# Optimization experiments

Hardware: AMD Instinct MI355X
Metric: run time of the kernel (lower is better)

Reference implementation:

```python
import jax, jax.numpy as jnp
import numpy as np

N = 100000      # nodes
E = 1600000     # directed edges (avg degree 16)
D_IN, D_H, D_OUT = 128, 128, 64


def glorot(k, fi, fo):
    s = (6.0 / (fi + fo)) ** 0.5
    return jax.random.uniform(k, (fi, fo), jnp.float32, -s, s)


def setup_inputs() -> dict:
    key = jax.random.key(0)
    ks = jax.random.split(key, 5)
    edges = jax.random.randint(ks[0], (2, E), 0, N)
    features = jax.random.normal(ks[1], (N, D_IN), dtype=jnp.float32)
    return dict(
        edges=edges,
        features=features,
        W0=glorot(ks[2], D_IN, D_H), b0=jnp.zeros((D_H,), jnp.float32),
        W1=glorot(ks[3], D_H, D_H), b1=jnp.zeros((D_H,), jnp.float32),
        W2=glorot(ks[4], D_H, D_OUT), b2=jnp.zeros((D_OUT,), jnp.float32),
    )


def _prep(edges):
    # add self-loops and compute symmetric GCN normalization D^-1/2 A_hat D^-1/2
    loop = jnp.arange(N)
    row = jnp.concatenate([edges[0], loop])  # source
    col = jnp.concatenate([edges[1], loop])  # target
    deg = jax.ops.segment_sum(jnp.ones((row.shape[0],), jnp.float32), col, num_segments=N)
    dinv = jnp.where(deg > 0, jax.lax.rsqrt(deg), 0.0)
    norm = dinv[row] * dinv[col]             # per-edge coefficient
    return row, col, norm


def gcn_conv(x, row, col, norm, W, b):
    x = x @ W                                 # [N, out]
    msg = x[row] * norm[:, None]              # gather + scale, [E+N, out]
    return jax.ops.segment_sum(msg, col, num_segments=N) + b


def reference(edges, features, W0, b0, W1, b1, W2, b2):
    row, col, norm = _prep(edges)
    h = jax.nn.relu(gcn_conv(features, row, col, norm, W0, b0))
    h = jax.nn.relu(gcn_conv(h, row, col, norm, W1, b1))
    h = gcn_conv(h, row, col, norm, W2, b2)
    return jax.nn.log_softmax(h, axis=1)
```

## Files before the change

### kernel.cpp

```cpp
#include <hip/hip_runtime.h>
#include <hip/hip_bf16.h>
#include <math.h>

#define NN 100000
#define EE 1600000
#define NB2 391
#define NPART 256
#define CAP 4736

typedef __attribute__((ext_vector_type(8))) short short8;
typedef __attribute__((ext_vector_type(4))) float f32x4;
typedef __attribute__((ext_vector_type(2))) float f32x2;

__device__ inline unsigned short f2bf(float x) {
    unsigned u = __float_as_uint(x);
    unsigned r = u + 0x7FFFu + ((u >> 16) & 1u);
    return (unsigned short)(r >> 16);
}
__device__ inline unsigned pack2bf(float a, float b) {
    return (unsigned)f2bf(a) | ((unsigned)f2bf(b) << 16);
}
__device__ inline f32x2 bf2f2(unsigned u) {
    f32x2 r;
    r.x = __uint_as_float(u << 16);
    r.y = __uint_as_float(u & 0xFFFF0000u);
    return r;
}


__global__ void prep_weights(const float* __restrict__ W0, const float* __restrict__ W1,
                             const float* __restrict__ W2, unsigned short* __restrict__ Wt0,
                             unsigned short* __restrict__ Wt1, unsigned short* __restrict__ Wt2,
                             int* __restrict__ bcount) {
    int g = blockIdx.x * 256 + threadIdx.x;
    if (g < NB2) bcount[g] = 0;
    if (g < 16384) {
        int n = g >> 7, k = g & 127;
        Wt0[g] = f2bf(W0[k * 128 + n]);
    } else if (g < 32768) {
        int i = g - 16384;
        int n = i >> 7, k = i & 127;
        Wt1[i] = f2bf(W1[k * 128 + n]);
    } else if (g < 40960) {
        int i = g - 32768;
        int n = i >> 7, k = i & 127;
        Wt2[i] = f2bf(W2[k * 64 + n]);
    }
}


__global__ __launch_bounds__(256) void scatter_bump(const int* __restrict__ src,
                                                    const int* __restrict__ dst,
                                                    int* __restrict__ bcount,
                                                    int* __restrict__ P, int e) {
    __shared__ int cnt[NB2];
    __shared__ int basep[NB2];
    __shared__ int cur[NB2];
    int t = threadIdx.x;
    for (int i = t; i < NB2; i += 256) { cnt[i] = 0; cur[i] = 0; }
    __syncthreads();
    int chunk = (e + NPART - 1) / NPART;
    int b0 = blockIdx.x * chunk, b1 = min(e, b0 + chunk);
    for (int i = b0 + t; i < b1; i += 256)
        atomicAdd(&cnt[dst[i] >> 8], 1);
    __syncthreads();
    for (int i = t; i < NB2; i += 256) {
        int c = cnt[i];
        basep[i] = c ? atomicAdd(&bcount[i], c) : 0;
    }
    __syncthreads();
    for (int i = b0 + t; i < b1; i += 256) {
        int d = dst[i];
        int b = d >> 8;
        int p = basep[b] + atomicAdd(&cur[b], 1);
        P[(size_t)b * CAP + p] = (src[i] << 8) | (d & 255);
    }
}

__global__ __launch_bounds__(256) void bucket_build(const int* __restrict__ P,
                                                    const int* __restrict__ bcount,
                                                    int2* __restrict__ offs2,
                                                    float* __restrict__ dinv,
                                                    int* __restrict__ csr, int n) {
    __shared__ int cnt[256];
    __shared__ int sc[256];
    __shared__ int cur[256];
    __shared__ int stage[CAP];
    int b = blockIdx.x, t = threadIdx.x;
    int base = b * CAP;
    int count = bcount[b];
    cnt[t] = 0;
    __syncthreads();
    for (int i = t; i < count; i += 256)
        atomicAdd(&cnt[P[base + i] & 255], 1);
    __syncthreads();
    int v = cnt[t];
    sc[t] = v;
    for (int d = 1; d < 256; d <<= 1) {
        __syncthreads();
        int x = (t >= d) ? sc[t - d] : 0;
        __syncthreads();
        sc[t] += x;
    }
    __syncthreads();
    int myoff = sc[t] - v;
    int node = b * 256 + t;
    if (node < n) {
        offs2[node] = make_int2(base + myoff, base + myoff + v);
        dinv[node] = 1.0f / sqrtf((float)(v + 1));
    }
    cur[t] = myoff;
    __syncthreads();
    for (int i = t; i < count; i += 256) {
        int pe = P[base + i];
        int p = atomicAdd(&cur[pe & 255], 1);
        stage[p] = ((unsigned)pe) >> 8;
    }
    __syncthreads();
    for (int i = t; i < count; i += 256) csr[base + i] = stage[i];
}

template <int DOUT, bool A_IS_F32>
__global__ __launch_bounds__(256) void gemm_mfma(const void* __restrict__ Aptr,
                                                 const unsigned short* __restrict__ Wt,
                                                 const float* __restrict__ dinv,
                                                 unsigned short* __restrict__ Y, int nrows) {
    constexpr int KP = 136;
    constexpr int NT = DOUT / 16;
    __shared__ unsigned short sA[128 * KP];
    __shared__ unsigned short sB[DOUT * KP];
    const int row0 = blockIdx.x * 128;
    const int tid = threadIdx.x;

    for (int i = tid; i < DOUT * 16; i += 256) {
        int n = i >> 4, c = (i & 15) * 8;
        uint4 v = *(const uint4*)(Wt + n * 128 + c);
        *(uint4*)(&sB[n * KP + c]) = v;
    }
    if (A_IS_F32) {
        const float* A = (const float*)Aptr;
        for (int i = tid; i < 128 * 32; i += 256) {
            int r = i >> 5, c = (i & 31) * 4;
            float4 v = make_float4(0.f, 0.f, 0.f, 0.f);
            if (row0 + r < nrows) v = *(const float4*)(A + (size_t)(row0 + r) * 128 + c);
            uint2 o;
            o.x = pack2bf(v.x, v.y);
            o.y = pack2bf(v.z, v.w);
            *(uint2*)(&sA[r * KP + c]) = o;
        }
    } else {
        const unsigned short* A = (const unsigned short*)Aptr;
        for (int i = tid; i < 128 * 16; i += 256) {
            int r = i >> 4, c = (i & 15) * 8;
            uint4 v = make_uint4(0u, 0u, 0u, 0u);
            if (row0 + r < nrows) v = *(const uint4*)(A + (size_t)(row0 + r) * 128 + c);
            *(uint4*)(&sA[r * KP + c]) = v;
        }
    }
    __syncthreads();

    const int wave = tid >> 6;
    const int lane = tid & 63;
    const int m0 = lane & 15;
    const int kq = (lane >> 4) * 8;

    f32x4 acc[2][NT];
#pragma unroll
    for (int rt = 0; rt < 2; ++rt)
#pragma unroll
        for (int t = 0; t < NT; ++t) acc[rt][t] = (f32x4){0.f, 0.f, 0.f, 0.f};

#pragma unroll
    for (int k0 = 0; k0 < 128; k0 += 32) {
        short8 a0 = *(const short8*)(&sA[(wave * 32 + m0) * KP + k0 + kq]);
        short8 a1 = *(const short8*)(&sA[(wave * 32 + 16 + m0) * KP + k0 + kq]);
#pragma unroll
        for (int t = 0; t < NT; ++t) {
            short8 b = *(const short8*)(&sB[(t * 16 + m0) * KP + k0 + kq]);
            acc[0][t] = __builtin_amdgcn_mfma_f32_16x16x32_bf16(a0, b, acc[0][t], 0, 0, 0);
            acc[1][t] = __builtin_amdgcn_mfma_f32_16x16x32_bf16(a1, b, acc[1][t], 0, 0, 0);
        }
    }

#pragma unroll
    for (int rt = 0; rt < 2; ++rt)
#pragma unroll
        for (int r = 0; r < 4; ++r) {
            int row = row0 + wave * 32 + rt * 16 + (lane >> 4) * 4 + r;
            if (row < nrows) {
                float dv = dinv[row];
#pragma unroll
                for (int t = 0; t < NT; ++t)
                    Y[(size_t)row * DOUT + t * 16 + (lane & 15)] = f2bf(acc[rt][t][r] * dv);
            }
        }
}

__global__ __launch_bounds__(256) void agg128_bf16(const unsigned short* __restrict__ Xp,
                                                   const int* __restrict__ csr,
                                                   const int2* __restrict__ offs2,
                                                   const float* __restrict__ dinv,
                                                   const float* __restrict__ bias,
                                                   unsigned short* __restrict__ Y, int n) {
    __shared__ int sIdx[4][64];
    int wv = threadIdx.x >> 6;
    int node = blockIdx.x * 4 + wv;
    if (node >= n) return;
    int lane = threadIdx.x & 63;
    int q = lane >> 4;
    int l = lane & 15;
    int2 se = offs2[node];
    int s = se.x, deg = se.y - se.x;
    if (lane < deg) sIdx[wv][lane] = csr[s + lane];
    int dcap = min(deg, 64);
    const int* idx = sIdx[wv];
    f32x2 a0 = {0.f, 0.f}, a1 = {0.f, 0.f}, a2 = {0.f, 0.f}, a3 = {0.f, 0.f};
    int j = q;
    for (; j + 12 < dcap; j += 16) {
        int s0 = idx[j], s1 = idx[j + 4], s2 = idx[j + 8], s3 = idx[j + 12];
        uint4 u0 = *(const uint4*)(Xp + (size_t)s0 * 128 + l * 8);
        uint4 u1 = *(const uint4*)(Xp + (size_t)s1 * 128 + l * 8);
        uint4 u2 = *(const uint4*)(Xp + (size_t)s2 * 128 + l * 8);
        uint4 u3 = *(const uint4*)(Xp + (size_t)s3 * 128 + l * 8);
        a0 += bf2f2(u0.x); a1 += bf2f2(u0.y); a2 += bf2f2(u0.z); a3 += bf2f2(u0.w);
        a0 += bf2f2(u1.x); a1 += bf2f2(u1.y); a2 += bf2f2(u1.z); a3 += bf2f2(u1.w);
        a0 += bf2f2(u2.x); a1 += bf2f2(u2.y); a2 += bf2f2(u2.z); a3 += bf2f2(u2.w);
        a0 += bf2f2(u3.x); a1 += bf2f2(u3.y); a2 += bf2f2(u3.z); a3 += bf2f2(u3.w);
    }
    for (; j < dcap; j += 4) {
        int s0 = idx[j];
        uint4 u = *(const uint4*)(Xp + (size_t)s0 * 128 + l * 8);
        a0 += bf2f2(u.x); a1 += bf2f2(u.y); a2 += bf2f2(u.z); a3 += bf2f2(u.w);
    }
    for (int p = s + 64 + q; p < s + deg; p += 4) {
        int s0 = csr[p];
        uint4 u = *(const uint4*)(Xp + (size_t)s0 * 128 + l * 8);
        a0 += bf2f2(u.x); a1 += bf2f2(u.y); a2 += bf2f2(u.z); a3 += bf2f2(u.w);
    }
    if (q == 0) {
        uint4 u = *(const uint4*)(Xp + (size_t)node * 128 + l * 8);
        a0 += bf2f2(u.x); a1 += bf2f2(u.y); a2 += bf2f2(u.z); a3 += bf2f2(u.w);
    }
    float r0 = a0.x, r1 = a0.y, r2 = a1.x, r3 = a1.y;
    float r4 = a2.x, r5 = a2.y, r6 = a3.x, r7 = a3.y;
    r0 += __shfl_xor(r0, 16); r0 += __shfl_xor(r0, 32);
    r1 += __shfl_xor(r1, 16); r1 += __shfl_xor(r1, 32);
    r2 += __shfl_xor(r2, 16); r2 += __shfl_xor(r2, 32);
    r3 += __shfl_xor(r3, 16); r3 += __shfl_xor(r3, 32);
    r4 += __shfl_xor(r4, 16); r4 += __shfl_xor(r4, 32);
    r5 += __shfl_xor(r5, 16); r5 += __shfl_xor(r5, 32);
    r6 += __shfl_xor(r6, 16); r6 += __shfl_xor(r6, 32);
    r7 += __shfl_xor(r7, 16); r7 += __shfl_xor(r7, 32);
    if (q == 0) {
        float di = dinv[node];
        float4 bA = *(const float4*)(bias + l * 8);
        float4 bB = *(const float4*)(bias + l * 8 + 4);
        r0 = fmaxf(fmaf(di, r0, bA.x), 0.f); r1 = fmaxf(fmaf(di, r1, bA.y), 0.f);
        r2 = fmaxf(fmaf(di, r2, bA.z), 0.f); r3 = fmaxf(fmaf(di, r3, bA.w), 0.f);
        r4 = fmaxf(fmaf(di, r4, bB.x), 0.f); r5 = fmaxf(fmaf(di, r5, bB.y), 0.f);
        r6 = fmaxf(fmaf(di, r6, bB.z), 0.f); r7 = fmaxf(fmaf(di, r7, bB.w), 0.f);
        uint4 o;
        o.x = pack2bf(r0, r1); o.y = pack2bf(r2, r3);
        o.z = pack2bf(r4, r5); o.w = pack2bf(r6, r7);
        *(uint4*)(Y + (size_t)node * 128 + l * 8) = o;
    }
}

__global__ __launch_bounds__(256) void agg_softmax64_bf16(const unsigned short* __restrict__ Xp,
                                                          const int* __restrict__ csr,
                                                          const int2* __restrict__ offs2,
                                                          const float* __restrict__ dinv,
                                                          const float* __restrict__ bias,
                                                          float* __restrict__ out, int n) {
    __shared__ int sIdx[4][64];
    int wv = threadIdx.x >> 6;
    int node = blockIdx.x * 4 + wv;
    if (node >= n) return;
    int lane = threadIdx.x & 63;
    int g8 = lane >> 3;
    int l = lane & 7;
    int2 se = offs2[node];
    int s = se.x, deg = se.y - se.x;
    if (lane < deg) sIdx[wv][lane] = csr[s + lane];
    int dcap = min(deg, 64);
    const int* idx = sIdx[wv];
    f32x2 a0 = {0.f, 0.f}, a1 = {0.f, 0.f}, a2 = {0.f, 0.f}, a3 = {0.f, 0.f};
    int j = g8;
    for (; j + 8 < dcap; j += 16) {
        int s0 = idx[j], s1 = idx[j + 8];
        uint4 u0 = *(const uint4*)(Xp + (size_t)s0 * 64 + l * 8);
        uint4 u1 = *(const uint4*)(Xp + (size_t)s1 * 64 + l * 8);
        a0 += bf2f2(u0.x); a1 += bf2f2(u0.y); a2 += bf2f2(u0.z); a3 += bf2f2(u0.w);
        a0 += bf2f2(u1.x); a1 += bf2f2(u1.y); a2 += bf2f2(u1.z); a3 += bf2f2(u1.w);
    }
    if (j < dcap) {
        int s0 = idx[j];
        uint4 u = *(const uint4*)(Xp + (size_t)s0 * 64 + l * 8);
        a0 += bf2f2(u.x); a1 += bf2f2(u.y); a2 += bf2f2(u.z); a3 += bf2f2(u.w);
    }
    for (int p = s + 64 + g8; p < s + deg; p += 8) {
        int s0 = csr[p];
        uint4 u = *(const uint4*)(Xp + (size_t)s0 * 64 + l * 8);
        a0 += bf2f2(u.x); a1 += bf2f2(u.y); a2 += bf2f2(u.z); a3 += bf2f2(u.w);
    }
    if (g8 == 0) {
        uint4 u = *(const uint4*)(Xp + (size_t)node * 64 + l * 8);
        a0 += bf2f2(u.x); a1 += bf2f2(u.y); a2 += bf2f2(u.z); a3 += bf2f2(u.w);
    }
    float r0 = a0.x, r1 = a0.y, r2 = a1.x, r3 = a1.y;
    float r4 = a2.x, r5 = a2.y, r6 = a3.x, r7 = a3.y;
    r0 += __shfl_xor(r0, 8); r0 += __shfl_xor(r0, 16); r0 += __shfl_xor(r0, 32);
    r1 += __shfl_xor(r1, 8); r1 += __shfl_xor(r1, 16); r1 += __shfl_xor(r1, 32);
    r2 += __shfl_xor(r2, 8); r2 += __shfl_xor(r2, 16); r2 += __shfl_xor(r2, 32);
    r3 += __shfl_xor(r3, 8); r3 += __shfl_xor(r3, 16); r3 += __shfl_xor(r3, 32);
    r4 += __shfl_xor(r4, 8); r4 += __shfl_xor(r4, 16); r4 += __shfl_xor(r4, 32);
    r5 += __shfl_xor(r5, 8); r5 += __shfl_xor(r5, 16); r5 += __shfl_xor(r5, 32);
    r6 += __shfl_xor(r6, 8); r6 += __shfl_xor(r6, 16); r6 += __shfl_xor(r6, 32);
    r7 += __shfl_xor(r7, 8); r7 += __shfl_xor(r7, 16); r7 += __shfl_xor(r7, 32);
    if (g8 == 0) {
        float di = dinv[node];
        float4 bA = *(const float4*)(bias + l * 8);
        float4 bB = *(const float4*)(bias + l * 8 + 4);
        r0 = fmaf(di, r0, bA.x); r1 = fmaf(di, r1, bA.y);
        r2 = fmaf(di, r2, bA.z); r3 = fmaf(di, r3, bA.w);
        r4 = fmaf(di, r4, bB.x); r5 = fmaf(di, r5, bB.y);
        r6 = fmaf(di, r6, bB.z); r7 = fmaf(di, r7, bB.w);
        float m = fmaxf(fmaxf(fmaxf(r0, r1), fmaxf(r2, r3)), fmaxf(fmaxf(r4, r5), fmaxf(r6, r7)));
#pragma unroll
        for (int o = 4; o > 0; o >>= 1) m = fmaxf(m, __shfl_xor(m, o));
        float ssum = __expf(r0 - m) + __expf(r1 - m) + __expf(r2 - m) + __expf(r3 - m) +
                     __expf(r4 - m) + __expf(r5 - m) + __expf(r6 - m) + __expf(r7 - m);
#pragma unroll
        for (int o = 4; o > 0; o >>= 1) ssum += __shfl_xor(ssum, o);
        float lg = m + __logf(ssum);
        float4 o0 = make_float4(r0 - lg, r1 - lg, r2 - lg, r3 - lg);
        float4 o1 = make_float4(r4 - lg, r5 - lg, r6 - lg, r7 - lg);
        *(float4*)(out + (size_t)node * 64 + l * 8) = o0;
        *(float4*)(out + (size_t)node * 64 + l * 8 + 4) = o1;
    }
}


extern "C" void kernel_launch(void* const* d_in, const int* in_sizes, int n_in,
                              void* d_out, int out_size, void* d_ws, size_t ws_size,
                              hipStream_t stream) {
    const int* edges = (const int*)d_in[0];
    const float* feat = (const float*)d_in[1];
    const float* W0 = (const float*)d_in[2];
    const float* b0 = (const float*)d_in[3];
    const float* W1 = (const float*)d_in[4];
    const float* b1 = (const float*)d_in[5];
    const float* W2 = (const float*)d_in[6];
    const float* b2 = (const float*)d_in[7];

    const int N = NN;
    const int E = EE;

    char* ws = (char*)d_ws;
    int* bcount = (int*)ws;
    int2* offs2 = (int2*)(bcount + ((NB2 + 1) & ~1));
    float* dinv = (float*)(offs2 + N);
    int* P = (int*)(dinv + N);
    int* csr = P + (size_t)NB2 * CAP;
    unsigned short* Wt0 = (unsigned short*)(csr + (size_t)NB2 * CAP);
    unsigned short* Wt1 = Wt0 + 16384;
    unsigned short* Wt2 = Wt1 + 16384;
    size_t off = (size_t)((char*)(Wt2 + 8192) - ws);
    off = (off + 255) & ~(size_t)255;
    unsigned short* bufA = (unsigned short*)(ws + off);
    unsigned short* bufB = bufA + (size_t)N * 128;

    const int* esrc = edges;
    const int* edst = edges + E;

    prep_weights<<<160, 256, 0, stream>>>(W0, W1, W2, Wt0, Wt1, Wt2, bcount);
    scatter_bump<<<NPART, 256, 0, stream>>>(esrc, edst, bcount, P, E);
    bucket_build<<<NB2, 256, 0, stream>>>(P, bcount, offs2, dinv, csr, N);

    const int gemmBlocks = (N + 127) / 128;
    const int aggBlocks = (N + 3) / 4;

    gemm_mfma<128, true><<<gemmBlocks, 256, 0, stream>>>(feat, Wt0, dinv, bufA, N);
    agg128_bf16<<<aggBlocks, 256, 0, stream>>>(bufA, csr, offs2, dinv, b0, bufB, N);
    gemm_mfma<128, false><<<gemmBlocks, 256, 0, stream>>>(bufB, Wt1, dinv, bufA, N);
    agg128_bf16<<<aggBlocks, 256, 0, stream>>>(bufA, csr, offs2, dinv, b1, bufB, N);
    gemm_mfma<64, false><<<gemmBlocks, 256, 0, stream>>>(bufB, Wt2, dinv, bufA, N);
    agg_softmax64_bf16<<<aggBlocks, 256, 0, stream>>>(bufA, csr, offs2, dinv, b2, (float*)d_out, N);
}
```

Measured before the change: 394.7 us.

## Store hidden features in 16-column slices so aggregation gathers fit cache

Hidden activations for the 128-wide layers are now laid out as 8 column slices of 16 bf16 values per node, each slice a contiguous N×16 array. The GEMM writes and reads this sliced layout, and the aggregation kernel launches 8× more blocks, each handling a single slice for 4 nodes. Each slice (about 3.2MB) is small enough to stay resident in L2/LLC during the random neighbour gathers. The cost is 8× redundant CSR/offset reads and index staging, 8-byte gathers instead of 16-byte ones, and more shuffle-reduction steps.

```diff
diff --git a/kernel.cpp b/kernel.cpp
--- a/kernel.cpp
+++ b/kernel.cpp
@@ -7,6 +7,7 @@
 #define NB2 391
 #define NPART 256
 #define CAP 4736
+#define SLS ((size_t)NN * 16)
 
 typedef __attribute__((ext_vector_type(8))) short short8;
 typedef __attribute__((ext_vector_type(4))) float f32x4;
@@ -120,7 +121,7 @@
     for (int i = t; i < count; i += 256) csr[base + i] = stage[i];
 }
 
-template <int DOUT, bool A_IS_F32>
+template <int DOUT, bool A_IS_F32, bool Y_SLICED>
 __global__ __launch_bounds__(256) void gemm_mfma(const void* __restrict__ Aptr,
                                                  const unsigned short* __restrict__ Wt,
                                                  const float* __restrict__ dinv,
@@ -151,10 +152,12 @@
     } else {
         const unsigned short* A = (const unsigned short*)Aptr;
         for (int i = tid; i < 128 * 16; i += 256) {
-            int r = i >> 4, c = (i & 15) * 8;
+            int r = i >> 4, c8 = (i & 15) * 8;
+            int sl = c8 >> 4, inner = c8 & 15;
             uint4 v = make_uint4(0u, 0u, 0u, 0u);
-            if (row0 + r < nrows) v = *(const uint4*)(A + (size_t)(row0 + r) * 128 + c);
-            *(uint4*)(&sA[r * KP + c]) = v;
+            if (row0 + r < nrows)
+                v = *(const uint4*)(A + (size_t)sl * SLS + (size_t)(row0 + r) * 16 + inner);
+            *(uint4*)(&sA[r * KP + c8]) = v;
         }
     }
     __syncthreads();
@@ -190,8 +193,13 @@
             if (row < nrows) {
                 float dv = dinv[row];
 #pragma unroll
-                for (int t = 0; t < NT; ++t)
-                    Y[(size_t)row * DOUT + t * 16 + (lane & 15)] = f2bf(acc[rt][t][r] * dv);
+                for (int t = 0; t < NT; ++t) {
+                    unsigned short val = f2bf(acc[rt][t][r] * dv);
+                    if (Y_SLICED)
+                        Y[(size_t)t * SLS + (size_t)row * 16 + (lane & 15)] = val;
+                    else
+                        Y[(size_t)row * DOUT + t * 16 + (lane & 15)] = val;
+                }
             }
         }
 }
@@ -203,66 +211,62 @@
                                                    const float* __restrict__ bias,
                                                    unsigned short* __restrict__ Y, int n) {
     __shared__ int sIdx[4][64];
+    int slice = blockIdx.x & 7;
+    int group = blockIdx.x >> 3;
     int wv = threadIdx.x >> 6;
-    int node = blockIdx.x * 4 + wv;
+    int node = group * 4 + wv;
     if (node >= n) return;
     int lane = threadIdx.x & 63;
-    int q = lane >> 4;
-    int l = lane & 15;
+    int sub = lane >> 2;
+    int l = lane & 3;
     int2 se = offs2[node];
     int s = se.x, deg = se.y - se.x;
     if (lane < deg) sIdx[wv][lane] = csr[s + lane];
     int dcap = min(deg, 64);
     const int* idx = sIdx[wv];
-    f32x2 a0 = {0.f, 0.f}, a1 = {0.f, 0.f}, a2 = {0.f, 0.f}, a3 = {0.f, 0.f};
-    int j = q;
-    for (; j + 12 < dcap; j += 16) {
-        int s0 = idx[j], s1 = idx[j + 4], s2 = idx[j + 8], s3 = idx[j + 12];
-        uint4 u0 = *(const uint4*)(Xp + (size_t)s0 * 128 + l * 8);
-        uint4 u1 = *(const uint4*)(Xp + (size_t)s1 * 128 + l * 8);
-        uint4 u2 = *(const uint4*)(Xp + (size_t)s2 * 128 + l * 8);
-        uint4 u3 = *(const uint4*)(Xp + (size_t)s3 * 128 + l * 8);
-        a0 += bf2f2(u0.x); a1 += bf2f2(u0.y); a2 += bf2f2(u0.z); a3 += bf2f2(u0.w);
-        a0 += bf2f2(u1.x); a1 += bf2f2(u1.y); a2 += bf2f2(u1.z); a3 += bf2f2(u1.w);
-        a0 += bf2f2(u2.x); a1 += bf2f2(u2.y); a2 += bf2f2(u2.z); a3 += bf2f2(u2.w);
-        a0 += bf2f2(u3.x); a1 += bf2f2(u3.y); a2 += bf2f2(u3.z); a3 += bf2f2(u3.w);
-    }
-    for (; j < dcap; j += 4) {
+    const unsigned short* Xs = Xp + (size_t)slice * SLS;
+    f32x2 a0 = {0.f, 0.f}, a1 = {0.f, 0.f};
+    int j = sub;
+    for (; j + 16 < dcap; j += 32) {
+        int s0 = idx[j], s1 = idx[j + 16];
+        uint2 u0 = *(const uint2*)(Xs + (size_t)s0 * 16 + l * 4);
+        uint2 u1 = *(const uint2*)(Xs + (size_t)s1 * 16 + l * 4);
+        a0 += bf2f2(u0.x); a1 += bf2f2(u0.y);
+        a0 += bf2f2(u1.x); a1 += bf2f2(u1.y);
+    }
+    if (j < dcap) {
         int s0 = idx[j];
-        uint4 u = *(const uint4*)(Xp + (size_t)s0 * 128 + l * 8);
-        a0 += bf2f2(u.x); a1 += bf2f2(u.y); a2 += bf2f2(u.z); a3 += bf2f2(u.w);
-    }
-    for (int p = s + 64 + q; p < s + deg; p += 4) {
+        uint2 u = *(const uint2*)(Xs + (size_t)s0 * 16 + l * 4);
+        a0 += bf2f2(u.x); a1 += bf2f2(u.y);
+    }
+    for (int p = s + 64 + sub; p < s + deg; p += 16) {
         int s0 = csr[p];
-        uint4 u = *(const uint4*)(Xp + (size_t)s0 * 128 + l * 8);
-        a0 += bf2f2(u.x); a1 += bf2f2(u.y); a2 += bf2f2(u.z); a3 += bf2f2(u.w);
-    }
-    if (q == 0) {
-        uint4 u = *(const uint4*)(Xp + (size_t)node * 128 + l * 8);
-        a0 += bf2f2(u.x); a1 += bf2f2(u.y); a2 += bf2f2(u.z); a3 += bf2f2(u.w);
+        uint2 u = *(const uint2*)(Xs + (size_t)s0 * 16 + l * 4);
+        a0 += bf2f2(u.x); a1 += bf2f2(u.y);
+    }
+    if (sub == 0) {
+        uint2 u = *(const uint2*)(Xs + (size_t)node * 16 + l * 4);
+        a0 += bf2f2(u.x); a1 += bf2f2(u.y);
     }
     float r0 = a0.x, r1 = a0.y, r2 = a1.x, r3 = a1.y;
-    float r4 = a2.x, r5 = a2.y, r6 = a3.x, r7 = a3.y;
-    r0 += __shfl_xor(r0, 16); r0 += __shfl_xor(r0, 32);
-    r1 += __shfl_xor(r1, 16); r1 += __shfl_xor(r1, 32);
-    r2 += __shfl_xor(r2, 16); r2 += __shfl_xor(r2, 32);
-    r3 += __shfl_xor(r3, 16); r3 += __shfl_xor(r3, 32);
-    r4 += __shfl_xor(r4, 16); r4 += __shfl_xor(r4, 32);
-    r5 += __shfl_xor(r5, 16); r5 += __shfl_xor(r5, 32);
-    r6 += __shfl_xor(r6, 16); r6 += __shfl_xor(r6, 32);
-    r7 += __shfl_xor(r7, 16); r7 += __shfl_xor(r7, 32);
-    if (q == 0) {
+#pragma unroll
+    for (int o = 4; o < 64; o <<= 1) {
+        r0 += __shfl_xor(r0, o);
+        r1 += __shfl_xor(r1, o);
+        r2 += __shfl_xor(r2, o);
+        r3 += __shfl_xor(r3, o);
+    }
+    if (sub == 0) {
         float di = dinv[node];
-        float4 bA = *(const float4*)(bias + l * 8);
-        float4 bB = *(const float4*)(bias + l * 8 + 4);
-        r0 = fmaxf(fmaf(di, r0, bA.x), 0.f); r1 = fmaxf(fmaf(di, r1, bA.y), 0.f);
-        r2 = fmaxf(fmaf(di, r2, bA.z), 0.f); r3 = fmaxf(fmaf(di, r3, bA.w), 0.f);
-        r4 = fmaxf(fmaf(di, r4, bB.x), 0.f); r5 = fmaxf(fmaf(di, r5, bB.y), 0.f);
-        r6 = fmaxf(fmaf(di, r6, bB.z), 0.f); r7 = fmaxf(fmaf(di, r7, bB.w), 0.f);
-        uint4 o;
-        o.x = pack2bf(r0, r1); o.y = pack2bf(r2, r3);
-        o.z = pack2bf(r4, r5); o.w = pack2bf(r6, r7);
-        *(uint4*)(Y + (size_t)node * 128 + l * 8) = o;
+        float4 b = *(const float4*)(bias + slice * 16 + l * 4);
+        r0 = fmaxf(fmaf(di, r0, b.x), 0.f);
+        r1 = fmaxf(fmaf(di, r1, b.y), 0.f);
+        r2 = fmaxf(fmaf(di, r2, b.z), 0.f);
+        r3 = fmaxf(fmaf(di, r3, b.w), 0.f);
+        uint2 o;
+        o.x = pack2bf(r0, r1);
+        o.y = pack2bf(r2, r3);
+        *(uint2*)(Y + (size_t)slice * SLS + (size_t)node * 16 + l * 4) = o;
     }
 }
 
@@ -378,12 +382,13 @@
     bucket_build<<<NB2, 256, 0, stream>>>(P, bcount, offs2, dinv, csr, N);
 
     const int gemmBlocks = (N + 127) / 128;
-    const int aggBlocks = (N + 3) / 4;
-
-    gemm_mfma<128, true><<<gemmBlocks, 256, 0, stream>>>(feat, Wt0, dinv, bufA, N);
-    agg128_bf16<<<aggBlocks, 256, 0, stream>>>(bufA, csr, offs2, dinv, b0, bufB, N);
-    gemm_mfma<128, false><<<gemmBlocks, 256, 0, stream>>>(bufB, Wt1, dinv, bufA, N);
-    agg128_bf16<<<aggBlocks, 256, 0, stream>>>(bufA, csr, offs2, dinv, b1, bufB, N);
-    gemm_mfma<64, false><<<gemmBlocks, 256, 0, stream>>>(bufB, Wt2, dinv, bufA, N);
-    agg_softmax64_bf16<<<aggBlocks, 256, 0, stream>>>(bufA, csr, offs2, dinv, b2, (float*)d_out, N);
-}
+    const int aggGroups = (N + 3) / 4;
+    const int aggBlocks128 = aggGroups * 8;
+
+    gemm_mfma<128, true, true><<<gemmBlocks, 256, 0, stream>>>(feat, Wt0, dinv, bufA, N);
+    agg128_bf16<<<aggBlocks128, 256, 0, stream>>>(bufA, csr, offs2, dinv, b0, bufB, N);
+    gemm_mfma<128, false, true><<<gemmBlocks, 256, 0, stream>>>(bufB, Wt1, dinv, bufA, N);
+    agg128_bf16<<<aggBlocks128, 256, 0, stream>>>(bufA, csr, offs2, dinv, b1, bufB, N);
+    gemm_mfma<64, false, false><<<gemmBlocks, 256, 0, stream>>>(bufB, Wt2, dinv, bufA, N);
+    agg_softmax64_bf16<<<aggGroups, 256, 0, stream>>>(bufA, csr, offs2, dinv, b2, (float*)d_out, N);
+}
```

Measured after the change: 741.8 us. 88.0% more time.
